# Kernel optimization log

Hardware: AMD Instinct MI355X
Metric: run time of the kernel (lower is better)

Reference implementation:

```python
import jax, jax.numpy as jnp
import numpy as np

LN_EPS = 1e-5      # torch layer_norm default eps
L2_EPS = 1e-12     # torch F.normalize default eps
SM_EPS = 1e-12
TAU = 1.0          # self.tau set in __init__
ROW_FLOOR = 0.05
ROW_CEILING = 0.35
NEG = -1e9


def _layer_norm(z):
    m = z.mean(axis=-1, keepdims=True)
    v = z.var(axis=-1, keepdims=True)
    return (z - m) / jnp.sqrt(v + LN_EPS)


def _l2_normalize(z):
    n = jnp.sqrt(jnp.sum(z * z, axis=-1, keepdims=True))
    return z / jnp.maximum(n, L2_EPS)


def setup_inputs() -> dict:
    key = jax.random.key(0)
    k1, k2, k3, k4, k5 = jax.random.split(key, 5)
    B, N, T, C, H = 16, 128, 512, 64, 64
    gain = 1.414
    bound = gain * np.sqrt(6.0 / (C + H))  # xavier_uniform with gain
    x = jax.random.normal(k1, (B, N, T, C), dtype=jnp.float32)
    Wq = jax.random.uniform(k2, (H, C), minval=-bound, maxval=bound, dtype=jnp.float32)
    Wk = jax.random.uniform(k3, (H, C), minval=-bound, maxval=bound, dtype=jnp.float32)
    bq = jax.random.uniform(k4, (H,), minval=-0.1, maxval=0.1, dtype=jnp.float32)
    bk = jax.random.uniform(k5, (H,), minval=-0.1, maxval=0.1, dtype=jnp.float32)
    return {"x": x, "Wq": Wq, "bq": bq, "Wk": Wk, "bk": bk, "band": 2}


def reference(x, Wq, bq, Wk, bk, band):
    B, N, T, C = x.shape
    x_mean = x.mean(axis=1)  # (B, T, C) -- reduce over nodes
    Q = _l2_normalize(_layer_norm(x_mean @ Wq.T + bq))  # (B, T, H)
    K = _l2_normalize(_layer_norm(x_mean @ Wk.T + bk))  # (B, T, H)
    logits = jnp.clip(jnp.einsum('bth,bsh->bts', Q, K), -6.0, 6.0)  # (B, T, T)

    idx = jnp.arange(T)
    dist = jnp.abs(idx[None, :] - idx[:, None])
    mask = (dist <= band) & (dist > 0)  # self_loop=False removes diagonal

    masked = jnp.where(mask[None, :, :], logits, NEG)
    masked = masked - jnp.max(masked, axis=-1, keepdims=True)
    A = jax.nn.softmax(masked / TAU, axis=-1)
    A = jnp.maximum(A, SM_EPS)
    A = (1.0 - ROW_FLOOR) * A + ROW_FLOOR / T
    A = jnp.minimum(A, ROW_CEILING)
    A = A / jnp.maximum(jnp.sum(A, axis=-1, keepdims=True), SM_EPS)
    A = A / jnp.maximum(jnp.sum(A, axis=-1, keepdims=True), SM_EPS)
    return A, logits
```

## Files before the change

### kernel.cpp

```cpp
#include <hip/hip_runtime.h>
#include <math.h>

#define BB 16
#define NN 128
#define TT 512
#define CC 64
#define HH 64

typedef float f4v __attribute__((ext_vector_type(4)));

__device__ __forceinline__ float wsum64(float v) {
#pragma unroll
  for (int m = 1; m < 64; m <<= 1) v += __shfl_xor(v, m, 64);
  return v;
}

__global__ __launch_bounds__(256) void mean_kernel(
    const float* __restrict__ x, float* __restrict__ xmean) {
  const int tid = threadIdx.x;
  const int b = blockIdx.x >> 7;
  const int t0 = (blockIdx.x & 127) << 2;
  const int w = tid >> 6;
  const int lane = tid & 63;
  const int j = lane >> 4;
  const int c4 = lane & 15;

  const f4v* xp = (const f4v*)x;
  size_t base4 = ((size_t)b * NN * TT + (size_t)(t0 + j)) * 16 + c4 +
                 (size_t)(w * 32) * (TT * 16);
  f4v s = {0.f, 0.f, 0.f, 0.f};
#pragma unroll 16
  for (int n = 0; n < 32; ++n) {
    s += __builtin_nontemporal_load(&xp[base4 + (size_t)n * (TT * 16)]);
  }

  __shared__ float red[4][4][64];
  *(f4v*)&red[w][j][c4 * 4] = s;
  __syncthreads();

  const int jj = tid >> 6, cc = tid & 63;
  float m = (red[0][jj][cc] + red[1][jj][cc] + red[2][jj][cc] +
             red[3][jj][cc]) * (1.f / 128.f);
  xmean[((size_t)b * TT + t0 + jj) * CC + cc] = m;
}

__global__ __launch_bounds__(256) void proj_kernel(
    const float* __restrict__ xmean, const float* __restrict__ Wq,
    const float* __restrict__ bq, const float* __restrict__ Wk,
    const float* __restrict__ bk, float* __restrict__ Qt,
    float* __restrict__ Kmat) {
  __shared__ float Wq_s[64 * 65];
  __shared__ float Wk_s[64 * 65];
  __shared__ float xm_s[16 * 64];
  __shared__ float qt_s[64 * 17];

  const int tid = threadIdx.x;
  const int b = blockIdx.x >> 5;
  const int t0 = (blockIdx.x & 31) << 4;

#pragma unroll
  for (int it = 0; it < 16; ++it) {
    int i = it * 256 + tid;
    int h = i >> 6, c = i & 63;
    Wq_s[c * 65 + h] = Wq[i];
    Wk_s[c * 65 + h] = Wk[i];
  }
  ((float4*)xm_s)[tid] = ((const float4*)(xmean + ((size_t)b * TT + t0) * CC))[tid];
  __syncthreads();

  const int rw = tid >> 6;
  const int h = tid & 63;
  float qa[4], ka[4];
  const float bqv = bq[h], bkv = bk[h];
#pragma unroll
  for (int r = 0; r < 4; ++r) { qa[r] = bqv; ka[r] = bkv; }
#pragma unroll
  for (int c = 0; c < 64; ++c) {
    float wq = Wq_s[c * 65 + h];
    float wk = Wk_s[c * 65 + h];
#pragma unroll
    for (int r = 0; r < 4; ++r) {
      float xv = xm_s[(rw * 4 + r) * 64 + c];
      qa[r] = fmaf(xv, wq, qa[r]);
      ka[r] = fmaf(xv, wk, ka[r]);
    }
  }

#pragma unroll
  for (int r = 0; r < 4; ++r) {
    const int t = t0 + rw * 4 + r;
    float mq = wsum64(qa[r]) * (1.f / 64.f);
    float dq = qa[r] - mq;
    float vq = wsum64(dq * dq) * (1.f / 64.f);
    float yq = dq / sqrtf(vq + 1e-5f);
    float nq = sqrtf(wsum64(yq * yq));
    yq = yq / fmaxf(nq, 1e-12f);
    qt_s[h * 17 + rw * 4 + r] = yq;

    float mk = wsum64(ka[r]) * (1.f / 64.f);
    float dk = ka[r] - mk;
    float vk = wsum64(dk * dk) * (1.f / 64.f);
    float yk = dk / sqrtf(vk + 1e-5f);
    float nk = sqrtf(wsum64(yk * yk));
    yk = yk / fmaxf(nk, 1e-12f);
    Kmat[((size_t)b * TT + t) * HH + h] = yk;
  }
  __syncthreads();

  {
    const int hh = tid >> 2, part = tid & 3;
    float4 o;
    o.x = qt_s[hh * 17 + part * 4 + 0];
    o.y = qt_s[hh * 17 + part * 4 + 1];
    o.z = qt_s[hh * 17 + part * 4 + 2];
    o.w = qt_s[hh * 17 + part * 4 + 3];
    *(float4*)&Qt[((size_t)b * HH + hh) * TT + t0 + part * 4] = o;
  }
}

__global__ __launch_bounds__(256) void logits_kernel(
    const float* __restrict__ Qt, const float* __restrict__ Kmat,
    float* __restrict__ logits) {
  __shared__ float Ks[256 * 65];

  const int tid = threadIdx.x;
  const int lane = tid & 63;
  const int w = tid >> 6;
  const int b = blockIdx.x >> 6;
  const int rem = blockIdx.x & 63;
  const int rg = rem >> 1;
  const int half = rem & 1;
  const int r0 = rg * 16;
  const int cbase = half * 256;

  {
    const float4* kg = (const float4*)(Kmat + ((size_t)b * TT + cbase) * HH);
#pragma unroll 8
    for (int it = 0; it < 64; ++it) {
      int g = it * 256 + tid;
      float4 v = kg[g];
      int row = g >> 4, h0 = (g & 15) * 4;
      float* d = &Ks[row * 65 + h0];
      d[0] = v.x; d[1] = v.y; d[2] = v.z; d[3] = v.w;
    }
  }
  __syncthreads();

  float acc[16];
#pragma unroll
  for (int r = 0; r < 16; ++r) acc[r] = 0.f;

  const float* krow = &Ks[(w * 64 + lane) * 65];
  const float* qtb = Qt + (size_t)b * HH * TT + r0;
#pragma unroll
  for (int c4 = 0; c4 < 16; ++c4) {
    float kx = krow[c4 * 4 + 0];
    float ky = krow[c4 * 4 + 1];
    float kz = krow[c4 * 4 + 2];
    float kw = krow[c4 * 4 + 3];
    const float* q0 = qtb + (size_t)(4 * c4 + 0) * TT;
    const float* q1 = qtb + (size_t)(4 * c4 + 1) * TT;
    const float* q2 = qtb + (size_t)(4 * c4 + 2) * TT;
    const float* q3 = qtb + (size_t)(4 * c4 + 3) * TT;
#pragma unroll
    for (int r = 0; r < 16; ++r) {
      acc[r] = fmaf(q0[r], kx, acc[r]);
      acc[r] = fmaf(q1[r], ky, acc[r]);
      acc[r] = fmaf(q2[r], kz, acc[r]);
      acc[r] = fmaf(q3[r], kw, acc[r]);
    }
  }

  float* lrow = logits + ((size_t)b * TT + r0) * TT + cbase + w * 64 + lane;
#pragma unroll
  for (int r = 0; r < 16; ++r) {
    float v = fminf(fmaxf(acc[r], -6.f), 6.f);
    lrow[(size_t)r * TT] = v;
  }
}

__global__ __launch_bounds__(256) void adj_kernel(
    const float* __restrict__ logits, const int* __restrict__ bandp,
    float* __restrict__ A) {
  const int w = threadIdx.x >> 6, lane = threadIdx.x & 63;
  const int row = blockIdx.x * 4 + w;
  const int t = row & (TT - 1);
  const int band = *bandp;
  const float* lrow = logits + (size_t)row * TT;

  float mx = -3.0e38f;
  for (int jj = -band; jj <= band; ++jj) {
    if (jj == 0) continue;
    int ss = t + jj;
    if (ss < 0 || ss >= TT) continue;
    mx = fmaxf(mx, lrow[ss]);
  }
  float den = 0.f;
  int nb = 0;
  for (int jj = -band; jj <= band; ++jj) {
    if (jj == 0) continue;
    int ss = t + jj;
    if (ss < 0 || ss >= TT) continue;
    den += expf(lrow[ss] - mx);
    ++nb;
  }
  const float fl = 0.05f / (float)TT;
  const float offa = 0.95f * 1e-12f + fl;
  float bsum = 0.f;
  for (int jj = -band; jj <= band; ++jj) {
    if (jj == 0) continue;
    int ss = t + jj;
    if (ss < 0 || ss >= TT) continue;
    float p = expf(lrow[ss] - mx) / den;
    float a = fminf(0.95f * p + fl, 0.35f);
    bsum += a;
  }
  const float s1 = fmaxf(bsum + (float)(TT - nb) * offa, 1e-12f);
  const float off1 = offa / s1;
  float bsum1 = 0.f;
  for (int jj = -band; jj <= band; ++jj) {
    if (jj == 0) continue;
    int ss = t + jj;
    if (ss < 0 || ss >= TT) continue;
    float p = expf(lrow[ss] - mx) / den;
    float a = fminf(0.95f * p + fl, 0.35f);
    bsum1 += a / s1;
  }
  const float s2 = fmaxf(bsum1 + (float)(TT - nb) * off1, 1e-12f);
  const float off2 = off1 / s2;

  auto colval = [&](int ss) -> float {
    int d = ss - t;
    if (d != 0 && d >= -band && d <= band) {
      float p = expf(lrow[ss] - mx) / den;
      float a = fminf(0.95f * p + fl, 0.35f);
      return a / s1 / s2;
    }
    return off2;
  };

  float* arow = A + (size_t)row * TT + lane * 8;
  const int cb = lane * 8;
  float4 o0, o1;
  o0.x = colval(cb + 0); o0.y = colval(cb + 1);
  o0.z = colval(cb + 2); o0.w = colval(cb + 3);
  o1.x = colval(cb + 4); o1.y = colval(cb + 5);
  o1.z = colval(cb + 6); o1.w = colval(cb + 7);
  *(float4*)&arow[0] = o0;
  *(float4*)&arow[4] = o1;
}

extern "C" void kernel_launch(void* const* d_in, const int* in_sizes, int n_in,
                              void* d_out, int out_size, void* d_ws, size_t ws_size,
                              hipStream_t stream) {
  (void)in_sizes; (void)n_in; (void)out_size; (void)ws_size;
  const float* x  = (const float*)d_in[0];
  const float* Wq = (const float*)d_in[1];
  const float* bq = (const float*)d_in[2];
  const float* Wk = (const float*)d_in[3];
  const float* bk = (const float*)d_in[4];
  const int* band = (const int*)d_in[5];

  float* A = (float*)d_out;
  float* logits = A + (size_t)BB * TT * TT;
  float* xmean = (float*)d_ws;
  float* Qt = xmean + (size_t)BB * TT * CC;
  float* Kmat = Qt + (size_t)BB * HH * TT;

  mean_kernel<<<2048, 256, 0, stream>>>(x, xmean);
  proj_kernel<<<512, 256, 0, stream>>>(xmean, Wq, bq, Wk, bk, Qt, Kmat);
  logits_kernel<<<1024, 256, 0, stream>>>(Qt, Kmat, logits);
  adj_kernel<<<2048, 256, 0, stream>>>(logits, band, A);
}
```

Measured before the change: 104.9 us.

## Fuse mean with projection and logits with adjacency into two kernels

Merges the node-mean and Q/K projection kernels so the mean stays in shared memory, and merges the logits GEMM with the banded softmax/adjacency step so A is built from in-block band values without re-reading logits from memory. Cuts four launches to two and removes the xmean round trip and the logits re-read. In exchange, each projection block now reloads and transposes both weight matrices for only 4 rows, and the fused logits kernel runs 512 blocks with serial per-row softmax done by 16 threads. Band handling is capped at 8.

```diff
diff --git a/kernel.cpp b/kernel.cpp
--- a/kernel.cpp
+++ b/kernel.cpp
@@ -15,90 +15,81 @@
   return v;
 }
 
-__global__ __launch_bounds__(256) void mean_kernel(
-    const float* __restrict__ x, float* __restrict__ xmean) {
-  const int tid = threadIdx.x;
-  const int b = blockIdx.x >> 7;
-  const int t0 = (blockIdx.x & 127) << 2;
-  const int w = tid >> 6;
-  const int lane = tid & 63;
-  const int j = lane >> 4;
-  const int c4 = lane & 15;
-
-  const f4v* xp = (const f4v*)x;
-  size_t base4 = ((size_t)b * NN * TT + (size_t)(t0 + j)) * 16 + c4 +
-                 (size_t)(w * 32) * (TT * 16);
-  f4v s = {0.f, 0.f, 0.f, 0.f};
-#pragma unroll 16
-  for (int n = 0; n < 32; ++n) {
-    s += __builtin_nontemporal_load(&xp[base4 + (size_t)n * (TT * 16)]);
-  }
-
-  __shared__ float red[4][4][64];
-  *(f4v*)&red[w][j][c4 * 4] = s;
-  __syncthreads();
-
-  const int jj = tid >> 6, cc = tid & 63;
-  float m = (red[0][jj][cc] + red[1][jj][cc] + red[2][jj][cc] +
-             red[3][jj][cc]) * (1.f / 128.f);
-  xmean[((size_t)b * TT + t0 + jj) * CC + cc] = m;
-}
-
-__global__ __launch_bounds__(256) void proj_kernel(
-    const float* __restrict__ xmean, const float* __restrict__ Wq,
+__global__ __launch_bounds__(256) void mean_proj_kernel(
+    const float* __restrict__ x, const float* __restrict__ Wq,
     const float* __restrict__ bq, const float* __restrict__ Wk,
     const float* __restrict__ bk, float* __restrict__ Qt,
     float* __restrict__ Kmat) {
   __shared__ float Wq_s[64 * 65];
   __shared__ float Wk_s[64 * 65];
-  __shared__ float xm_s[16 * 64];
-  __shared__ float qt_s[64 * 17];
+  __shared__ float red[4][4][64];
+  __shared__ float xm_s[4][64];
+  __shared__ float qt_s[64 * 5];
 
   const int tid = threadIdx.x;
-  const int b = blockIdx.x >> 5;
-  const int t0 = (blockIdx.x & 31) << 4;
-
-#pragma unroll
-  for (int it = 0; it < 16; ++it) {
-    int i = it * 256 + tid;
-    int h = i >> 6, c = i & 63;
-    Wq_s[c * 65 + h] = Wq[i];
-    Wk_s[c * 65 + h] = Wk[i];
-  }
-  ((float4*)xm_s)[tid] = ((const float4*)(xmean + ((size_t)b * TT + t0) * CC))[tid];
+  const int b = blockIdx.x >> 7;
+  const int t0 = (blockIdx.x & 127) << 2;
+
+  {
+    const float4* wq4 = (const float4*)Wq;
+    const float4* wk4 = (const float4*)Wk;
+#pragma unroll
+    for (int it = 0; it < 4; ++it) {
+      int i4 = it * 256 + tid;
+      float4 q = wq4[i4], k = wk4[i4];
+      int h = i4 >> 4, c0 = (i4 & 15) * 4;
+      Wq_s[(c0 + 0) * 65 + h] = q.x; Wq_s[(c0 + 1) * 65 + h] = q.y;
+      Wq_s[(c0 + 2) * 65 + h] = q.z; Wq_s[(c0 + 3) * 65 + h] = q.w;
+      Wk_s[(c0 + 0) * 65 + h] = k.x; Wk_s[(c0 + 1) * 65 + h] = k.y;
+      Wk_s[(c0 + 2) * 65 + h] = k.z; Wk_s[(c0 + 3) * 65 + h] = k.w;
+    }
+  }
+
+  {
+    const int w = tid >> 6;
+    const int lane = tid & 63;
+    const int j = lane >> 4;
+    const int c4 = lane & 15;
+    const f4v* xp = (const f4v*)x;
+    size_t base4 = ((size_t)b * NN * TT + (size_t)(t0 + j)) * 16 + c4 +
+                   (size_t)(w * 32) * (TT * 16);
+    f4v s = {0.f, 0.f, 0.f, 0.f};
+#pragma unroll 8
+    for (int n = 0; n < 32; ++n) {
+      s += xp[base4 + (size_t)n * (TT * 16)];
+    }
+    *(f4v*)&red[w][j][c4 * 4] = s;
+  }
+  __syncthreads();
+
+  {
+    const int jj = tid >> 6, cc = tid & 63;
+    xm_s[jj][cc] = (red[0][jj][cc] + red[1][jj][cc] + red[2][jj][cc] +
+                    red[3][jj][cc]) * (1.f / 128.f);
+  }
   __syncthreads();
 
   const int rw = tid >> 6;
   const int h = tid & 63;
-  float qa[4], ka[4];
-  const float bqv = bq[h], bkv = bk[h];
-#pragma unroll
-  for (int r = 0; r < 4; ++r) { qa[r] = bqv; ka[r] = bkv; }
+  float qa = bq[h], ka = bk[h];
 #pragma unroll
   for (int c = 0; c < 64; ++c) {
-    float wq = Wq_s[c * 65 + h];
-    float wk = Wk_s[c * 65 + h];
-#pragma unroll
-    for (int r = 0; r < 4; ++r) {
-      float xv = xm_s[(rw * 4 + r) * 64 + c];
-      qa[r] = fmaf(xv, wq, qa[r]);
-      ka[r] = fmaf(xv, wk, ka[r]);
-    }
-  }
-
-#pragma unroll
-  for (int r = 0; r < 4; ++r) {
-    const int t = t0 + rw * 4 + r;
-    float mq = wsum64(qa[r]) * (1.f / 64.f);
-    float dq = qa[r] - mq;
+    float xv = xm_s[rw][c];
+    qa = fmaf(xv, Wq_s[c * 65 + h], qa);
+    ka = fmaf(xv, Wk_s[c * 65 + h], ka);
+  }
+  {
+    const int t = t0 + rw;
+    float mq = wsum64(qa) * (1.f / 64.f);
+    float dq = qa - mq;
     float vq = wsum64(dq * dq) * (1.f / 64.f);
     float yq = dq / sqrtf(vq + 1e-5f);
     float nq = sqrtf(wsum64(yq * yq));
     yq = yq / fmaxf(nq, 1e-12f);
-    qt_s[h * 17 + rw * 4 + r] = yq;
-
-    float mk = wsum64(ka[r]) * (1.f / 64.f);
-    float dk = ka[r] - mk;
+    qt_s[h * 5 + rw] = yq;
+
+    float mk = wsum64(ka) * (1.f / 64.f);
+    float dk = ka - mk;
     float vk = wsum64(dk * dk) * (1.f / 64.f);
     float yk = dk / sqrtf(vk + 1e-5f);
     float nk = sqrtf(wsum64(yk * yk));
@@ -107,147 +98,156 @@
   }
   __syncthreads();
 
-  {
-    const int hh = tid >> 2, part = tid & 3;
+  if (tid < 64) {
     float4 o;
-    o.x = qt_s[hh * 17 + part * 4 + 0];
-    o.y = qt_s[hh * 17 + part * 4 + 1];
-    o.z = qt_s[hh * 17 + part * 4 + 2];
-    o.w = qt_s[hh * 17 + part * 4 + 3];
-    *(float4*)&Qt[((size_t)b * HH + hh) * TT + t0 + part * 4] = o;
-  }
-}
-
-__global__ __launch_bounds__(256) void logits_kernel(
+    o.x = qt_s[tid * 5 + 0]; o.y = qt_s[tid * 5 + 1];
+    o.z = qt_s[tid * 5 + 2]; o.w = qt_s[tid * 5 + 3];
+    *(float4*)&Qt[((size_t)b * HH + tid) * TT + t0] = o;
+  }
+}
+
+__global__ __launch_bounds__(256) void logits_adj_kernel(
     const float* __restrict__ Qt, const float* __restrict__ Kmat,
-    float* __restrict__ logits) {
-  __shared__ float Ks[256 * 65];
+    const int* __restrict__ bandp, float* __restrict__ logits,
+    float* __restrict__ A) {
+  __shared__ float Ks[128 * 68];
+  __shared__ float bandv[16][17];
+  __shared__ float finalA[16][17];
+  __shared__ float off2s[16];
 
   const int tid = threadIdx.x;
-  const int lane = tid & 63;
-  const int w = tid >> 6;
-  const int b = blockIdx.x >> 6;
-  const int rem = blockIdx.x & 63;
-  const int rg = rem >> 1;
-  const int half = rem & 1;
-  const int r0 = rg * 16;
-  const int cbase = half * 256;
-
-  {
-    const float4* kg = (const float4*)(Kmat + ((size_t)b * TT + cbase) * HH);
-#pragma unroll 8
-    for (int it = 0; it < 64; ++it) {
-      int g = it * 256 + tid;
-      float4 v = kg[g];
-      int row = g >> 4, h0 = (g & 15) * 4;
-      float* d = &Ks[row * 65 + h0];
-      d[0] = v.x; d[1] = v.y; d[2] = v.z; d[3] = v.w;
-    }
-  }
-  __syncthreads();
-
-  float acc[16];
-#pragma unroll
-  for (int r = 0; r < 16; ++r) acc[r] = 0.f;
-
-  const float* krow = &Ks[(w * 64 + lane) * 65];
-  const float* qtb = Qt + (size_t)b * HH * TT + r0;
-#pragma unroll
-  for (int c4 = 0; c4 < 16; ++c4) {
-    float kx = krow[c4 * 4 + 0];
-    float ky = krow[c4 * 4 + 1];
-    float kz = krow[c4 * 4 + 2];
-    float kw = krow[c4 * 4 + 3];
-    const float* q0 = qtb + (size_t)(4 * c4 + 0) * TT;
-    const float* q1 = qtb + (size_t)(4 * c4 + 1) * TT;
-    const float* q2 = qtb + (size_t)(4 * c4 + 2) * TT;
-    const float* q3 = qtb + (size_t)(4 * c4 + 3) * TT;
-#pragma unroll
-    for (int r = 0; r < 16; ++r) {
-      acc[r] = fmaf(q0[r], kx, acc[r]);
-      acc[r] = fmaf(q1[r], ky, acc[r]);
-      acc[r] = fmaf(q2[r], kz, acc[r]);
-      acc[r] = fmaf(q3[r], kw, acc[r]);
-    }
-  }
-
-  float* lrow = logits + ((size_t)b * TT + r0) * TT + cbase + w * 64 + lane;
-#pragma unroll
-  for (int r = 0; r < 16; ++r) {
-    float v = fminf(fmaxf(acc[r], -6.f), 6.f);
-    lrow[(size_t)r * TT] = v;
-  }
-}
-
-__global__ __launch_bounds__(256) void adj_kernel(
-    const float* __restrict__ logits, const int* __restrict__ bandp,
-    float* __restrict__ A) {
-  const int w = threadIdx.x >> 6, lane = threadIdx.x & 63;
-  const int row = blockIdx.x * 4 + w;
-  const int t = row & (TT - 1);
+  const int b = blockIdx.x >> 5;
+  const int r0 = (blockIdx.x & 31) << 4;
   const int band = *bandp;
-  const float* lrow = logits + (size_t)row * TT;
-
-  float mx = -3.0e38f;
-  for (int jj = -band; jj <= band; ++jj) {
-    if (jj == 0) continue;
-    int ss = t + jj;
-    if (ss < 0 || ss >= TT) continue;
-    mx = fmaxf(mx, lrow[ss]);
-  }
-  float den = 0.f;
-  int nb = 0;
-  for (int jj = -band; jj <= band; ++jj) {
-    if (jj == 0) continue;
-    int ss = t + jj;
-    if (ss < 0 || ss >= TT) continue;
-    den += expf(lrow[ss] - mx);
-    ++nb;
-  }
-  const float fl = 0.05f / (float)TT;
-  const float offa = 0.95f * 1e-12f + fl;
-  float bsum = 0.f;
-  for (int jj = -band; jj <= band; ++jj) {
-    if (jj == 0) continue;
-    int ss = t + jj;
-    if (ss < 0 || ss >= TT) continue;
-    float p = expf(lrow[ss] - mx) / den;
-    float a = fminf(0.95f * p + fl, 0.35f);
-    bsum += a;
-  }
-  const float s1 = fmaxf(bsum + (float)(TT - nb) * offa, 1e-12f);
-  const float off1 = offa / s1;
-  float bsum1 = 0.f;
-  for (int jj = -band; jj <= band; ++jj) {
-    if (jj == 0) continue;
-    int ss = t + jj;
-    if (ss < 0 || ss >= TT) continue;
-    float p = expf(lrow[ss] - mx) / den;
-    float a = fminf(0.95f * p + fl, 0.35f);
-    bsum1 += a / s1;
-  }
-  const float s2 = fmaxf(bsum1 + (float)(TT - nb) * off1, 1e-12f);
-  const float off2 = off1 / s2;
-
-  auto colval = [&](int ss) -> float {
-    int d = ss - t;
-    if (d != 0 && d >= -band && d <= band) {
-      float p = expf(lrow[ss] - mx) / den;
+  const int colL = tid & 127;
+
+  const float* qbase = Qt + (size_t)b * HH * TT + r0;
+
+  for (int chunk = 0; chunk < 4; ++chunk) {
+    const int cbase = chunk << 7;
+    {
+      const float4* kg = (const float4*)(Kmat + ((size_t)b * TT + cbase) * HH);
+#pragma unroll
+      for (int it = 0; it < 8; ++it) {
+        int g = it * 256 + tid;
+        float4 v = kg[g];
+        int row = g >> 4, h0 = (g & 15) * 4;
+        float* d = &Ks[row * 68 + h0];
+        d[0] = v.x; d[1] = v.y; d[2] = v.z; d[3] = v.w;
+      }
+    }
+    __syncthreads();
+
+    const int col = cbase + colL;
+    const float* kr = &Ks[colL * 68];
+
+    auto body = [&](int roff) {
+      float acc[8] = {0.f, 0.f, 0.f, 0.f, 0.f, 0.f, 0.f, 0.f};
+#pragma unroll
+      for (int h4 = 0; h4 < 16; ++h4) {
+        f4v k4 = *(const f4v*)&kr[h4 * 4];
+#pragma unroll
+        for (int j = 0; j < 4; ++j) {
+          const float* qr = qbase + (size_t)(h4 * 4 + j) * TT + roff;
+          float4 qlo = *(const float4*)qr;
+          float4 qhi = *(const float4*)(qr + 4);
+          float kk = k4[j];
+          acc[0] = fmaf(qlo.x, kk, acc[0]);
+          acc[1] = fmaf(qlo.y, kk, acc[1]);
+          acc[2] = fmaf(qlo.z, kk, acc[2]);
+          acc[3] = fmaf(qlo.w, kk, acc[3]);
+          acc[4] = fmaf(qhi.x, kk, acc[4]);
+          acc[5] = fmaf(qhi.y, kk, acc[5]);
+          acc[6] = fmaf(qhi.z, kk, acc[6]);
+          acc[7] = fmaf(qhi.w, kk, acc[7]);
+        }
+      }
+#pragma unroll
+      for (int r = 0; r < 8; ++r) {
+        const int rl = roff + r;
+        float v = fminf(fmaxf(acc[r], -6.f), 6.f);
+        __builtin_nontemporal_store(
+            v, &logits[((size_t)b * TT + r0 + rl) * TT + col]);
+        int d = col - (r0 + rl);
+        if (d != 0 && d >= -band && d <= band && d >= -8 && d <= 8)
+          bandv[rl][d + 8] = v;
+      }
+    };
+    if (tid < 128) body(0); else body(8);
+    __syncthreads();
+  }
+
+  if (tid < 16) {
+    const int rg = r0 + tid;
+    float mx = -3.0e38f;
+    for (int jj = -band; jj <= band; ++jj) {
+      if (jj == 0) continue;
+      int ss = rg + jj;
+      if (ss < 0 || ss >= TT || jj < -8 || jj > 8) continue;
+      mx = fmaxf(mx, bandv[tid][jj + 8]);
+    }
+    float den = 0.f;
+    int nb = 0;
+    for (int jj = -band; jj <= band; ++jj) {
+      if (jj == 0) continue;
+      int ss = rg + jj;
+      if (ss < 0 || ss >= TT || jj < -8 || jj > 8) continue;
+      den += expf(bandv[tid][jj + 8] - mx);
+      ++nb;
+    }
+    const float fl = 0.05f / (float)TT;
+    const float offa = 0.95f * 1e-12f + fl;
+    float bsum = 0.f;
+    for (int jj = -band; jj <= band; ++jj) {
+      if (jj == 0) continue;
+      int ss = rg + jj;
+      if (ss < 0 || ss >= TT || jj < -8 || jj > 8) continue;
+      float p = expf(bandv[tid][jj + 8] - mx) / den;
       float a = fminf(0.95f * p + fl, 0.35f);
-      return a / s1 / s2;
-    }
-    return off2;
-  };
-
-  float* arow = A + (size_t)row * TT + lane * 8;
-  const int cb = lane * 8;
-  float4 o0, o1;
-  o0.x = colval(cb + 0); o0.y = colval(cb + 1);
-  o0.z = colval(cb + 2); o0.w = colval(cb + 3);
-  o1.x = colval(cb + 4); o1.y = colval(cb + 5);
-  o1.z = colval(cb + 6); o1.w = colval(cb + 7);
-  *(float4*)&arow[0] = o0;
-  *(float4*)&arow[4] = o1;
+      bsum += a;
+    }
+    const float s1 = fmaxf(bsum + (float)(TT - nb) * offa, 1e-12f);
+    const float off1 = offa / s1;
+    float bsum1 = 0.f;
+    for (int jj = -band; jj <= band; ++jj) {
+      if (jj == 0) continue;
+      int ss = rg + jj;
+      if (ss < 0 || ss >= TT || jj < -8 || jj > 8) continue;
+      float p = expf(bandv[tid][jj + 8] - mx) / den;
+      float a = fminf(0.95f * p + fl, 0.35f);
+      bsum1 += a / s1;
+    }
+    const float s2 = fmaxf(bsum1 + (float)(TT - nb) * off1, 1e-12f);
+    const float off2 = off1 / s2;
+
+    for (int e = 0; e < 17; ++e) finalA[tid][e] = off2;
+    for (int jj = -band; jj <= band; ++jj) {
+      if (jj == 0) continue;
+      int ss = rg + jj;
+      if (ss < 0 || ss >= TT || jj < -8 || jj > 8) continue;
+      float p = expf(bandv[tid][jj + 8] - mx) / den;
+      float a = fminf(0.95f * p + fl, 0.35f);
+      finalA[tid][jj + 8] = a / s1 / s2;
+    }
+    off2s[tid] = off2;
+  }
+  __syncthreads();
+
+  const int half = tid >> 7;
+#pragma unroll
+  for (int chunk = 0; chunk < 4; ++chunk) {
+    const int col = (chunk << 7) + colL;
+#pragma unroll
+    for (int r = 0; r < 8; ++r) {
+      const int rl = half * 8 + r;
+      int d = col - (r0 + rl);
+      float v = (d >= -band && d <= band && d >= -8 && d <= 8)
+                    ? finalA[rl][d + 8]
+                    : off2s[rl];
+      __builtin_nontemporal_store(
+          v, &A[((size_t)b * TT + r0 + rl) * TT + col]);
+    }
+  }
 }
 
 extern "C" void kernel_launch(void* const* d_in, const int* in_sizes, int n_in,
@@ -263,12 +263,9 @@
 
   float* A = (float*)d_out;
   float* logits = A + (size_t)BB * TT * TT;
-  float* xmean = (float*)d_ws;
-  float* Qt = xmean + (size_t)BB * TT * CC;
+  float* Qt = (float*)d_ws;
   float* Kmat = Qt + (size_t)BB * HH * TT;
 
-  mean_kernel<<<2048, 256, 0, stream>>>(x, xmean);
-  proj_kernel<<<512, 256, 0, stream>>>(xmean, Wq, bq, Wk, bk, Qt, Kmat);
-  logits_kernel<<<1024, 256, 0, stream>>>(Qt, Kmat, logits);
-  adj_kernel<<<2048, 256, 0, stream>>>(logits, band, A);
-}
+  mean_proj_kernel<<<2048, 256, 0, stream>>>(x, Wq, bq, Wk, bk, Qt, Kmat);
+  logits_adj_kernel<<<512, 256, 0, stream>>>(Qt, Kmat, band, logits, A);
+}
```

Result: slower. 145.1 us (+38.4%).
